# Kernel tuning notes

Hardware: AMD Instinct MI355X
Metric: run time of the kernel (lower is better)

The kernel has to match this reference:

```python
import jax, jax.numpy as jnp
import numpy as np
from jax import lax

NPOINT = 1024
RADIUS = 0.2
NSAMPLE = 32
BN_EPS = 1e-3  # tf_util batch_norm variance_epsilon


def setup_inputs() -> dict:
    key = jax.random.key(0)
    ks = jax.random.split(key, 16)
    B, N, Cp = 8, 4096, 64
    mlp = [64, 64, 128]
    cin = 3 + Cp  # use_xyz=True concatenates local coords
    dk, dout = 128, 128
    inp = {}
    inp["xyz"] = jax.random.uniform(ks[0], (B, N, 3), jnp.float32)
    inp["points"] = jax.random.normal(ks[1], (B, N, Cp), jnp.float32)
    dims = [cin] + mlp
    for i in range(3):
        inp[f"W{i}"] = jax.random.normal(ks[2 + i], (dims[i], dims[i + 1]), jnp.float32) / np.sqrt(dims[i]).astype(np.float32)
        inp[f"b{i}"] = jnp.zeros((dims[i + 1],), jnp.float32)
        inp[f"g{i}"] = jnp.ones((dims[i + 1],), jnp.float32)
        inp[f"be{i}"] = jnp.zeros((dims[i + 1],), jnp.float32)
    inp["Wq"] = jax.random.normal(ks[10], (3, dk), jnp.float32) * 0.1
    inp["Wk"] = jax.random.normal(ks[11], (mlp[-1], dk), jnp.float32) * 0.1
    inp["Wv"] = jax.random.normal(ks[12], (mlp[-1], dout), jnp.float32) * 0.1
    return inp


def farthest_point_sample(xyz, npoint):
    # xyz: [B, N, 3] -> idx [B, npoint] (sequential FPS, seeded at point 0)
    B, N, _ = xyz.shape

    def body(carry, _):
        dist, farthest = carry  # dist [B,N], farthest [B]
        centroid = jnp.take_along_axis(xyz, farthest[:, None, None], axis=1)  # [B,1,3]
        d = jnp.sum((xyz - centroid) ** 2, axis=-1)  # [B,N]
        dist = jnp.minimum(dist, d)
        nxt = jnp.argmax(dist, axis=-1).astype(jnp.int32)
        return (dist, nxt), farthest

    init = (jnp.full((B, N), 1e10, xyz.dtype), jnp.zeros((B,), jnp.int32))
    _, idxs = lax.scan(body, init, None, length=npoint)
    return jnp.transpose(idxs)  # [B, npoint]


def query_ball_point(radius, nsample, xyz, new_xyz):
    # first `nsample` points (in index order) within radius; pad with first hit
    N = xyz.shape[1]
    d2 = jnp.sum((new_xyz[:, :, None, :] - xyz[:, None, :, :]) ** 2, axis=-1)  # [B,S,N]
    inball = d2 < radius * radius
    ar = jnp.arange(N, dtype=jnp.int32)
    order_key = jnp.where(inball, ar, ar + N)
    idx = jnp.argsort(order_key, axis=-1)[..., :nsample].astype(jnp.int32)  # [B,S,nsample]
    valid = jnp.take_along_axis(inball, idx, axis=-1)
    idx = jnp.where(valid, idx, idx[..., :1])
    return idx


def group_point(feat, idx):
    # feat [B,N,C], idx [B,S,K] -> [B,S,K,C]
    return jax.vmap(lambda f, i: f[i])(feat, idx)


def _conv_bn_relu(x, W, b, g, be):
    y = jnp.einsum('bskc,cd->bskd', x, W) + b  # 1x1 conv == pointwise linear
    mean = jnp.mean(y, axis=(0, 1, 2))
    var = jnp.var(y, axis=(0, 1, 2))
    y = (y - mean) * g * lax.rsqrt(var + BN_EPS) + be
    return jax.nn.relu(y)


def _forward(xyz, points, Ws, bs, gs, bes, Wq, Wk, Wv):
    fps_idx = farthest_point_sample(xyz, NPOINT)                 # [B,S]
    new_xyz = jnp.take_along_axis(xyz, fps_idx[..., None], 1)    # [B,S,3]
    idx = query_ball_point(RADIUS, NSAMPLE, xyz, new_xyz)        # [B,S,K]
    grouped_xyz = group_point(xyz, idx) - new_xyz[:, :, None, :]  # local coords
    grouped_pts = group_point(points, idx)
    new_points = jnp.concatenate([grouped_xyz, grouped_pts], axis=-1)  # [B,S,K,3+C]
    for W, b, g, be in zip(Ws, bs, gs, bes):
        new_points = _conv_bn_relu(new_points, W, b, g, be)
    # attention pooling over the K neighbors, query from group center coords
    dk = Wq.shape[1]
    q = new_xyz @ Wq                                         # [B,S,dk]
    k = jnp.einsum('bskc,cd->bskd', new_points, Wk)          # [B,S,K,dk]
    v = jnp.einsum('bskc,co->bsko', new_points, Wv)          # [B,S,K,out]
    scores = jax.nn.softmax(jnp.einsum('bsd,bskd->bsk', q, k) / jnp.sqrt(jnp.float32(dk)), axis=-1)
    pooled = jnp.einsum('bsk,bsko->bso', scores, v)          # [B,S,out]
    return new_xyz, pooled, idx


def reference(xyz, points, W0, b0, g0, be0, W1, b1, g1, be1, W2, b2, g2, be2, Wq, Wk, Wv):
    return _forward(xyz, points, (W0, W1, W2), (b0, b1, b2), (g0, g1, g2), (be0, be1, be2), Wq, Wk, Wv)
```

## Files before the change

kernel.cpp:

```cpp
#include <hip/hip_runtime.h>
#include <hip/hip_bf16.h>

#define DI __device__ __forceinline__

DI float fmulr(float a, float b){ return __fmul_rn(a,b); }
DI float faddr(float a, float b){ return __fadd_rn(a,b); }
DI float fsubr(float a, float b){ return __fsub_rn(a,b); }
DI float dist2e(float x,float y,float z,float cx,float cy,float cz){
  float dx=fsubr(x,cx), dy=fsubr(y,cy), dz=fsubr(z,cz);
  return faddr(faddr(fmulr(dx,dx),fmulr(dy,dy)),fmulr(dz,dz));
}
DI unsigned short f2bf(float f){ __hip_bfloat16 h=__float2bfloat16(f); return *reinterpret_cast<unsigned short*>(&h); }

template<int C> DI float dmax_step(float x){
  int y=__builtin_amdgcn_update_dpp(0, __float_as_int(x), C, 0xF, 0xF, true);
  return fmaxf(x, __int_as_float(y));
}

__global__ __launch_bounds__(256) void fps_kernel(const float* __restrict__ xyz, float* __restrict__ out0){
  __shared__ float4 sp4[4096];
  float* spf=(float*)sp4;
  int* spi=(int*)sp4;
  int b=blockIdx.x, tid=threadIdx.x;
  const float* xb = xyz + (size_t)b*4096*3;
  for(int e=tid;e<12288;e+=256){
    int p=e/3, c=e-3*p;
    spf[4*p+c]=xb[e];
  }
  __syncthreads();
  float px[16],py[16],pz[16],dist[16];
  int p0 = tid*16;
  #pragma unroll
  for(int j=0;j<16;j++){ float4 r=sp4[p0+j]; px[j]=r.x; py[j]=r.y; pz[j]=r.z; dist[j]=1e10f; }
  int cur=0;
  float4 cc0=sp4[0];
  float cx=cc0.x, cy=cc0.y, cz=cc0.z;
  int w=tid>>6, lane=tid&63;
  int c0s=0,c1s=0,c2s=0,c3s=0;
  float* ob = out0 + (size_t)b*1024*3;
  #pragma unroll 1
  for(int t=0;t<1024;t++){
    bool mine = ((t&255)==tid);
    int hi = t>>8;
    c0s = (mine && hi==0) ? cur : c0s;
    c1s = (mine && hi==1) ? cur : c1s;
    c2s = (mine && hi==2) ? cur : c2s;
    c3s = (mine && hi==3) ? cur : c3s;
    float nd[16];
    #pragma unroll
    for(int j=0;j<16;j++){
      float d=dist2e(px[j],py[j],pz[j],cx,cy,cz);
      float m=fminf(dist[j],d); dist[j]=m; nd[j]=m;
    }
    float a0=fmaxf(nd[0],nd[1]), a1=fmaxf(nd[2],nd[3]), a2=fmaxf(nd[4],nd[5]), a3=fmaxf(nd[6],nd[7]);
    float a4=fmaxf(nd[8],nd[9]), a5=fmaxf(nd[10],nd[11]), a6=fmaxf(nd[12],nd[13]), a7=fmaxf(nd[14],nd[15]);
    float b0=fmaxf(a0,a1), b1=fmaxf(a2,a3), b2=fmaxf(a4,a5), b3=fmaxf(a6,a7);
    float bv=fmaxf(fmaxf(b0,b1),fmaxf(b2,b3));
    unsigned msk=0u;
    #pragma unroll
    for(int j=0;j<16;j++) msk |= (nd[j]==bv) ? (1u<<j) : 0u;
    int bj=__ffs(msk)-1;
    int bi=p0+bj;
    float x=bv;
    x=dmax_step<0x111>(x); x=dmax_step<0x112>(x); x=dmax_step<0x114>(x); x=dmax_step<0x118>(x);
    x=dmax_step<0x142>(x); x=dmax_step<0x143>(x);
    float wv=__int_as_float(__builtin_amdgcn_readlane(__float_as_int(x),63));
    unsigned long long em=__ballot(bv==wv);
    int L=(int)(__ffsll(em)-1);
    int wbi=__builtin_amdgcn_readlane(bi,L);
    int par=t&1;
    if(lane==0){
      spf[4*(par*8+w)+3]=wv;
      spi[4*(par*8+4+w)+3]=wbi;
    }
    __syncthreads();
    float w0=spf[4*(par*8+0)+3], w1=spf[4*(par*8+1)+3], w2=spf[4*(par*8+2)+3], w3=spf[4*(par*8+3)+3];
    int   i0=spi[4*(par*8+4)+3], i1=spi[4*(par*8+5)+3], i2=spi[4*(par*8+6)+3], i3=spi[4*(par*8+7)+3];
    float mv=fmaxf(fmaxf(w0,w1),fmaxf(w2,w3));
    int u0=(w0==mv)?i0:0x7fffffff, u1=(w1==mv)?i1:0x7fffffff;
    int u2=(w2==mv)?i2:0x7fffffff, u3=(w3==mv)?i3:0x7fffffff;
    cur=min(min(u0,u1),min(u2,u3));
    float4 cc=sp4[cur]; cx=cc.x; cy=cc.y; cz=cc.z;
  }
  { int t0=tid;     float4 c=sp4[c0s]; ob[t0*3]=c.x; ob[t0*3+1]=c.y; ob[t0*3+2]=c.z; }
  { int t1=tid+256; float4 c=sp4[c1s]; ob[t1*3]=c.x; ob[t1*3+1]=c.y; ob[t1*3+2]=c.z; }
  { int t2=tid+512; float4 c=sp4[c2s]; ob[t2*3]=c.x; ob[t2*3+1]=c.y; ob[t2*3+2]=c.z; }
  { int t3=tid+768; float4 c=sp4[c3s]; ob[t3*3]=c.x; ob[t3*3+1]=c.y; ob[t3*3+2]=c.z; }
}

__global__ __launch_bounds__(256) void ballq_kernel(const float* __restrict__ xyz, const float* __restrict__ out0,
        int* __restrict__ idxw, float* __restrict__ out2){
  __shared__ float sp[12288];
  int tid=threadIdx.x;
  int g = blockIdx.x*4 + (tid>>6);
  int lane = tid&63;
  int b = blockIdx.x>>8;
  const float* xb = xyz + (size_t)b*4096*3;
  const float4* src=(const float4*)xb; float4* dst=(float4*)sp;
  #pragma unroll
  for(int i=0;i<12;i++) dst[i*256+tid]=src[i*256+tid];
  __syncthreads();
  float cx=out0[(size_t)g*3], cy=out0[(size_t)g*3+1], cz=out0[(size_t)g*3+2];
  const float R2 = (float)(0.2*0.2);
  int cnt=0, firstp=0; bool haveFirst=false;
  for(int c=0;c<64;c++){
    int p=c*64+lane;
    float x=sp[3*p], y=sp[3*p+1], z=sp[3*p+2];
    float d2=dist2e(x,y,z,cx,cy,cz);
    bool inb = d2 < R2;
    unsigned long long mask=__ballot(inb);
    if(!haveFirst && mask){ firstp = c*64 + (__ffsll((unsigned long long)mask)-1); haveFirst=true; }
    int pos = cnt + (int)__popcll(mask & ((1ull<<lane)-1ull));
    if(inb && pos<32){ idxw[(size_t)g*32+pos]=p; out2[(size_t)g*32+pos]=(float)p; }
    cnt += (int)__popcll(mask);
    if(cnt>=32) break;
  }
  if(cnt<32){
    for(int j=cnt+lane; j<32; j+=64){ idxw[(size_t)g*32+j]=firstp; out2[(size_t)g*32+j]=(float)firstp; }
  }
}

__global__ void m_kernel(const float* __restrict__ Wq, const float* __restrict__ Wk, float* __restrict__ M){
  int c = threadIdx.x;
  float m0=0.f,m1=0.f,m2=0.f;
  for(int d=0; d<128; d++){
    float wk = Wk[c*128+d];
    m0 += Wq[d]*wk; m1 += Wq[128+d]*wk; m2 += Wq[256+d]*wk;
  }
  M[c]=m0; M[128+c]=m1; M[256+c]=m2;
}

__global__ __launch_bounds__(256) void l0_kernel(const float* __restrict__ xyz, const float* __restrict__ pts,
    const float* __restrict__ out0, const int* __restrict__ idxw,
    const float* __restrict__ W0, const float* __restrict__ b0,
    __hip_bfloat16* __restrict__ y0, float* __restrict__ P){
  __shared__ float xl[64*69];
  int tid=threadIdx.x; int base=blockIdx.x*64;
  int w=tid>>6, lane=tid&63;
  for(int i=0;i<16;i++){
    int r=w*16+i; int R=base+r;
    int g=R>>5; int b=g>>10; int p=idxw[R];
    const float* prow = pts + ((size_t)b*4096 + (size_t)p)*64;
    xl[r*69+3+lane] = prow[lane];
    if(lane<3){
      xl[r*69+lane] = fsubr(xyz[((size_t)b*4096+(size_t)p)*3+lane], out0[(size_t)g*3+lane]);
    }
  }
  __syncthreads();
  int r=tid&63;
  int cgu=__builtin_amdgcn_readfirstlane(tid>>6);
  float acc[16];
  #pragma unroll
  for(int j=0;j<16;j++) acc[j]=b0[cgu*16+j];
  for(int c=0;c<67;c++){
    float xv=xl[r*69+c];
    #pragma unroll
    for(int j=0;j<16;j++) acc[j] += xv*W0[c*64+cgu*16+j];
  }
  size_t R=(size_t)base+r;
  unsigned short tb[16];
  #pragma unroll
  for(int j=0;j<16;j++) tb[j]=f2bf(acc[j]);
  uint4* ov=(uint4*)(y0 + R*64 + cgu*16);
  ov[0]=make_uint4(tb[0]|(tb[1]<<16), tb[2]|(tb[3]<<16), tb[4]|(tb[5]<<16), tb[6]|(tb[7]<<16));
  ov[1]=make_uint4(tb[8]|(tb[9]<<16), tb[10]|(tb[11]<<16), tb[12]|(tb[13]<<16), tb[14]|(tb[15]<<16));
  #pragma unroll
  for(int j=0;j<16;j++){
    float s=acc[j], q=acc[j]*acc[j];
    #pragma unroll
    for(int m=32;m>=1;m>>=1){ s+=__shfl_xor(s,m); q+=__shfl_xor(q,m); }
    if(r==0){ P[(size_t)(cgu*16+j)*4096 + blockIdx.x]=s; P[(size_t)(128+cgu*16+j)*4096 + blockIdx.x]=q; }
  }
}

template<int CIN,int COUT>
__global__ __launch_bounds__(256) void lmid_kernel(const __hip_bfloat16* __restrict__ xin,
    const float* __restrict__ ssIn, const float* __restrict__ W, const float* __restrict__ bias,
    __hip_bfloat16* __restrict__ yout, float* __restrict__ P){
  constexpr int STR=CIN+1;
  constexpr int PER=COUT/4;
  __shared__ float xl[64*STR];
  int tid=threadIdx.x; size_t base=(size_t)blockIdx.x*64;
  constexpr int CHUNKS = 64*CIN/8;
  #pragma unroll
  for(int i=0;i<CHUNKS/256;i++){
    int e=i*256+tid;
    int r=e/(CIN/8), c0=(e%(CIN/8))*8;
    uint4 raw = *reinterpret_cast<const uint4*>(xin + (base+(size_t)r)*CIN + c0);
    unsigned u[4]={raw.x,raw.y,raw.z,raw.w};
    #pragma unroll
    for(int k=0;k<4;k++){
      int c=c0+2*k;
      float lo=__uint_as_float(u[k]<<16);
      float hi=__uint_as_float(u[k]&0xFFFF0000u);
      float a=lo*ssIn[c]+ssIn[128+c];
      float bq=hi*ssIn[c+1]+ssIn[128+c+1];
      xl[r*STR+c]  = a>0.f?a:0.f;
      xl[r*STR+c+1]= bq>0.f?bq:0.f;
    }
  }
  __syncthreads();
  int r=tid&63;
  int cgu=__builtin_amdgcn_readfirstlane(tid>>6);
  float acc[PER];
  #pragma unroll
  for(int j=0;j<PER;j++) acc[j]=bias[cgu*PER+j];
  for(int c=0;c<CIN;c++){
    float xv=xl[r*STR+c];
    #pragma unroll
    for(int j=0;j<PER;j++) acc[j] += xv*W[c*COUT+cgu*PER+j];
  }
  size_t R=base+r;
  unsigned short tb[PER];
  #pragma unroll
  for(int j=0;j<PER;j++) tb[j]=f2bf(acc[j]);
  uint4* ov=(uint4*)(yout + R*COUT + cgu*PER);
  #pragma unroll
  for(int v=0;v<PER/8;v++)
    ov[v]=make_uint4(tb[v*8]|(tb[v*8+1]<<16), tb[v*8+2]|(tb[v*8+3]<<16), tb[v*8+4]|(tb[v*8+5]<<16), tb[v*8+6]|(tb[v*8+7]<<16));
  #pragma unroll
  for(int j=0;j<PER;j++){
    float s=acc[j],q=acc[j]*acc[j];
    #pragma unroll
    for(int m=32;m>=1;m>>=1){s+=__shfl_xor(s,m);q+=__shfl_xor(q,m);}
    if(r==0){ P[(size_t)(cgu*PER+j)*4096 + blockIdx.x]=s; P[(size_t)(128+cgu*PER+j)*4096 + blockIdx.x]=q; }
  }
}

__global__ void fin_kernel(const float* __restrict__ P, const float* __restrict__ gg, const float* __restrict__ be,
                           float* __restrict__ ss){
  int ch=blockIdx.x; int lane=threadIdx.x;
  float s=0.f,q=0.f;
  for(int blk=lane; blk<4096; blk+=64){ s+=P[(size_t)ch*4096+blk]; q+=P[(size_t)(128+ch)*4096+blk]; }
  #pragma unroll
  for(int m=32;m>=1;m>>=1){ s+=__shfl_xor(s,m); q+=__shfl_xor(q,m); }
  if(lane==0){
    const float invNT = 1.0f/262144.0f;
    float mean=s*invNT; float var=q*invNT - mean*mean;
    float scale=gg[ch]/sqrtf(var+1e-3f);
    ss[ch]=scale; ss[128+ch]=be[ch]-mean*scale;
  }
}

__global__ __launch_bounds__(256) void sh_kernel(const __hip_bfloat16* __restrict__ y2,
    const float* __restrict__ ss2, const float* __restrict__ M, const float* __restrict__ out0,
    float* __restrict__ hbar){
  __shared__ float h[2][32*130];
  __shared__ float uLds[2][128];
  __shared__ float sLds[2][32];
  int tid=threadIdx.x; int grp=tid>>7, t=tid&127;
  size_t g=(size_t)blockIdx.x*2+grp;
  #pragma unroll
  for(int i=0;i<4;i++){
    int e=i*128+t;
    int row=e>>4, c0=(e&15)*8;
    uint4 raw=*reinterpret_cast<const uint4*>(y2+(g*32+(size_t)row)*128+c0);
    unsigned u[4]={raw.x,raw.y,raw.z,raw.w};
    #pragma unroll
    for(int k=0;k<4;k++){
      int c=c0+2*k;
      float lo=__uint_as_float(u[k]<<16), hi=__uint_as_float(u[k]&0xFFFF0000u);
      float a=lo*ss2[c]+ss2[128+c]; float bq=hi*ss2[c+1]+ss2[128+c+1];
      h[grp][row*130+c]  = a>0.f?a:0.f;
      h[grp][row*130+c+1]= bq>0.f?bq:0.f;
    }
  }
  float cx=out0[g*3], cy=out0[g*3+1], cz=out0[g*3+2];
  uLds[grp][t]=cx*M[t]+cy*M[128+t]+cz*M[256+t];
  __syncthreads();
  if(t<32){
    float sc=0.f;
    for(int c=0;c<128;c++) sc+=h[grp][t*130+c]*uLds[grp][c];
    sc*=0.08838834764831845f;
    float mx=sc;
    #pragma unroll
    for(int m=16;m>=1;m>>=1) mx=fmaxf(mx,__shfl_xor(mx,m));
    float p=expf(sc-mx);
    float sum=p;
    #pragma unroll
    for(int m=16;m>=1;m>>=1) sum+=__shfl_xor(sum,m);
    sLds[grp][t]=p/sum;
  }
  __syncthreads();
  float hb=0.f;
  for(int k=0;k<32;k++) hb+=sLds[grp][k]*h[grp][k*130+t];
  hbar[g*128+t]=hb;
}

__global__ __launch_bounds__(256) void pool_kernel(const float* __restrict__ hbar, const float* __restrict__ Wv,
    float* __restrict__ out1){
  __shared__ float xl[32*129];
  int tid=threadIdx.x; size_t g0=(size_t)blockIdx.x*32;
  for(int e=tid;e<32*128;e+=256){ int r=e>>7,ch=e&127; xl[r*129+ch]=hbar[(g0+(size_t)r)*128+ch]; }
  __syncthreads();
  int r=tid&31;
  int cgu=__builtin_amdgcn_readfirstlane(tid>>5);
  float acc[16];
  #pragma unroll
  for(int j=0;j<16;j++) acc[j]=0.f;
  for(int c=0;c<128;c++){
    float xv=xl[r*129+c];
    #pragma unroll
    for(int j=0;j<16;j++) acc[j]+=xv*Wv[c*128+cgu*16+j];
  }
  #pragma unroll
  for(int j=0;j<16;j++) out1[(g0+(size_t)r)*128+cgu*16+j]=acc[j];
}

extern "C" void kernel_launch(void* const* d_in, const int* in_sizes, int n_in,
                              void* d_out, int out_size, void* d_ws, size_t ws_size,
                              hipStream_t stream){
  (void)in_sizes; (void)n_in; (void)out_size; (void)ws_size;
  const float* xyz=(const float*)d_in[0];
  const float* pts=(const float*)d_in[1];
  const float* W0=(const float*)d_in[2];  const float* b0=(const float*)d_in[3];
  const float* g0=(const float*)d_in[4];  const float* be0=(const float*)d_in[5];
  const float* W1=(const float*)d_in[6];  const float* b1=(const float*)d_in[7];
  const float* g1=(const float*)d_in[8];  const float* be1=(const float*)d_in[9];
  const float* W2=(const float*)d_in[10]; const float* b2=(const float*)d_in[11];
  const float* g2=(const float*)d_in[12]; const float* be2=(const float*)d_in[13];
  const float* Wq=(const float*)d_in[14]; const float* Wk=(const float*)d_in[15];
  const float* Wv=(const float*)d_in[16];
  float* out0=(float*)d_out;
  float* out1=out0 + (size_t)8*1024*3;
  float* out2=out1 + (size_t)8192*128;

  char* ws=(char*)d_ws; size_t off=0;
  int* idxw=(int*)(ws+off);                    off += (size_t)8192*32*4;
  __hip_bfloat16* fa=(__hip_bfloat16*)(ws+off); off += (size_t)262144*64*2;
  __hip_bfloat16* fb=(__hip_bfloat16*)(ws+off); off += (size_t)262144*64*2;
  __hip_bfloat16* fc=(__hip_bfloat16*)(ws+off); off += (size_t)262144*128*2;
  float* P =(float*)(ws+off);                  off += (size_t)256*4096*4;
  float* ss0=(float*)(ws+off);                 off += 256*4;
  float* ss1=(float*)(ws+off);                 off += 256*4;
  float* ss2=(float*)(ws+off);                 off += 256*4;
  float* M =(float*)(ws+off);                  off += 3*128*4 + 128;
  float* hb=(float*)(ws+off);                  off += (size_t)8192*128*4;

  hipLaunchKernelGGL(fps_kernel,   dim3(8),    dim3(256),  0, stream, xyz, out0);
  hipLaunchKernelGGL(ballq_kernel, dim3(2048), dim3(256),  0, stream, xyz, out0, idxw, out2);
  hipLaunchKernelGGL(m_kernel,     dim3(1),    dim3(128),  0, stream, Wq, Wk, M);
  hipLaunchKernelGGL(l0_kernel,    dim3(4096), dim3(256),  0, stream, xyz, pts, out0, idxw, W0, b0, fa, P);
  hipLaunchKernelGGL(fin_kernel,   dim3(64),   dim3(64),   0, stream, P, g0, be0, ss0);
  hipLaunchKernelGGL((lmid_kernel<64,64>),  dim3(4096), dim3(256), 0, stream, fa, ss0, W1, b1, fb, P);
  hipLaunchKernelGGL(fin_kernel,   dim3(64),   dim3(64),   0, stream, P, g1, be1, ss1);
  hipLaunchKernelGGL((lmid_kernel<64,128>), dim3(4096), dim3(256), 0, stream, fb, ss1, W2, b2, fc, P);
  hipLaunchKernelGGL(fin_kernel,   dim3(128),  dim3(64),   0, stream, P, g2, be2, ss2);
  hipLaunchKernelGGL(sh_kernel,    dim3(4096), dim3(256),  0, stream, fc, ss2, M, out0, hb);
  hipLaunchKernelGGL(pool_kernel,  dim3(256),  dim3(256),  0, stream, hb, Wv, out1);
}
```

Before: 970.7 us.

## Vectorize FPS distance update with packed float2 and pack argmax keys

The FPS inner loop now holds point coordinates in two-wide float vectors, so distance and min/max updates can map to packed FP32 instructions. FP contraction is turned off to keep results bitwise identical to the reference. The cross-wave argmax reduction packs value and inverted index into one 64-bit key in dedicated shared slots, replacing separate value and index reads and the tie-break logic with a plain integer max. Separately, the sh_kernel score dot product is split across four thread groups with partial sums in shared memory instead of 32 threads each looping over 128 channels, at the cost of an extra barrier.

```diff
diff --git a/kernel.cpp b/kernel.cpp
--- a/kernel.cpp
+++ b/kernel.cpp
@@ -2,6 +2,8 @@
 #include <hip/hip_bf16.h>
 
 #define DI __device__ __forceinline__
+
+typedef float v2f __attribute__((ext_vector_type(2)));
 
 DI float fmulr(float a, float b){ return __fmul_rn(a,b); }
 DI float faddr(float a, float b){ return __fadd_rn(a,b); }
@@ -18,9 +20,10 @@
 }
 
 __global__ __launch_bounds__(256) void fps_kernel(const float* __restrict__ xyz, float* __restrict__ out0){
-  __shared__ float4 sp4[4096];
-  float* spf=(float*)sp4;
-  int* spi=(int*)sp4;
+  extern __shared__ char smem[];
+  float4* sp4=(float4*)smem;
+  float* spf=(float*)smem;
+  unsigned long long* slots=(unsigned long long*)(smem+65536);
   int b=blockIdx.x, tid=threadIdx.x;
   const float* xb = xyz + (size_t)b*4096*3;
   for(int e=tid;e<12288;e+=256){
@@ -28,10 +31,14 @@
     spf[4*p+c]=xb[e];
   }
   __syncthreads();
-  float px[16],py[16],pz[16],dist[16];
-  int p0 = tid*16;
-  #pragma unroll
-  for(int j=0;j<16;j++){ float4 r=sp4[p0+j]; px[j]=r.x; py[j]=r.y; pz[j]=r.z; dist[j]=1e10f; }
+  v2f px[8],py[8],pz[8],dist[8];
+  int p0=tid*16;
+  #pragma unroll
+  for(int j=0;j<8;j++){
+    float4 r0=sp4[p0+2*j], r1=sp4[p0+2*j+1];
+    px[j]=(v2f){r0.x,r1.x}; py[j]=(v2f){r0.y,r1.y}; pz[j]=(v2f){r0.z,r1.z};
+    dist[j]=(v2f){1e10f,1e10f};
+  }
   int cur=0;
   float4 cc0=sp4[0];
   float cx=cc0.x, cy=cc0.y, cz=cc0.z;
@@ -40,25 +47,38 @@
   float* ob = out0 + (size_t)b*1024*3;
   #pragma unroll 1
   for(int t=0;t<1024;t++){
-    bool mine = ((t&255)==tid);
-    int hi = t>>8;
-    c0s = (mine && hi==0) ? cur : c0s;
-    c1s = (mine && hi==1) ? cur : c1s;
-    c2s = (mine && hi==2) ? cur : c2s;
-    c3s = (mine && hi==3) ? cur : c3s;
-    float nd[16];
-    #pragma unroll
-    for(int j=0;j<16;j++){
-      float d=dist2e(px[j],py[j],pz[j],cx,cy,cz);
-      float m=fminf(dist[j],d); dist[j]=m; nd[j]=m;
-    }
-    float a0=fmaxf(nd[0],nd[1]), a1=fmaxf(nd[2],nd[3]), a2=fmaxf(nd[4],nd[5]), a3=fmaxf(nd[6],nd[7]);
-    float a4=fmaxf(nd[8],nd[9]), a5=fmaxf(nd[10],nd[11]), a6=fmaxf(nd[12],nd[13]), a7=fmaxf(nd[14],nd[15]);
-    float b0=fmaxf(a0,a1), b1=fmaxf(a2,a3), b2=fmaxf(a4,a5), b3=fmaxf(a6,a7);
-    float bv=fmaxf(fmaxf(b0,b1),fmaxf(b2,b3));
+    bool mine=((t&255)==tid);
+    int hi=t>>8;
+    c0s=(mine&&hi==0)?cur:c0s;
+    c1s=(mine&&hi==1)?cur:c1s;
+    c2s=(mine&&hi==2)?cur:c2s;
+    c3s=(mine&&hi==3)?cur:c3s;
+    v2f nd[8];
+    {
+      #pragma clang fp contract(off)
+      v2f c2x={cx,cx}, c2y={cy,cy}, c2z={cz,cz};
+      #pragma unroll
+      for(int j=0;j<8;j++){
+        v2f dx=px[j]-c2x, dy=py[j]-c2y, dz=pz[j]-c2z;
+        v2f dd=(dx*dx+dy*dy)+dz*dz;
+        v2f nm=__builtin_elementwise_min(dist[j],dd);
+        dist[j]=nm; nd[j]=nm;
+      }
+    }
+    v2f e0=__builtin_elementwise_max(nd[0],nd[1]);
+    v2f e1=__builtin_elementwise_max(nd[2],nd[3]);
+    v2f e2=__builtin_elementwise_max(nd[4],nd[5]);
+    v2f e3=__builtin_elementwise_max(nd[6],nd[7]);
+    v2f f0=__builtin_elementwise_max(e0,e1);
+    v2f f1=__builtin_elementwise_max(e2,e3);
+    v2f g =__builtin_elementwise_max(f0,f1);
+    float bv=fmaxf(g.x,g.y);
     unsigned msk=0u;
     #pragma unroll
-    for(int j=0;j<16;j++) msk |= (nd[j]==bv) ? (1u<<j) : 0u;
+    for(int j=0;j<8;j++){
+      msk |= (nd[j].x==bv)?(1u<<(2*j)):0u;
+      msk |= (nd[j].y==bv)?(1u<<(2*j+1)):0u;
+    }
     int bj=__ffs(msk)-1;
     int bi=p0+bj;
     float x=bv;
@@ -70,16 +90,16 @@
     int wbi=__builtin_amdgcn_readlane(bi,L);
     int par=t&1;
     if(lane==0){
-      spf[4*(par*8+w)+3]=wv;
-      spi[4*(par*8+4+w)+3]=wbi;
+      slots[par*4+w] = ((unsigned long long)__float_as_uint(wv)<<32)
+                     | (unsigned long long)(0xFFFFFFFFu-(unsigned)wbi);
     }
     __syncthreads();
-    float w0=spf[4*(par*8+0)+3], w1=spf[4*(par*8+1)+3], w2=spf[4*(par*8+2)+3], w3=spf[4*(par*8+3)+3];
-    int   i0=spi[4*(par*8+4)+3], i1=spi[4*(par*8+5)+3], i2=spi[4*(par*8+6)+3], i3=spi[4*(par*8+7)+3];
-    float mv=fmaxf(fmaxf(w0,w1),fmaxf(w2,w3));
-    int u0=(w0==mv)?i0:0x7fffffff, u1=(w1==mv)?i1:0x7fffffff;
-    int u2=(w2==mv)?i2:0x7fffffff, u3=(w3==mv)?i3:0x7fffffff;
-    cur=min(min(u0,u1),min(u2,u3));
+    const ulonglong2* sl2=(const ulonglong2*)(slots+par*4);
+    ulonglong2 ka=sl2[0], kb=sl2[1];
+    unsigned long long m0 = ka.x>ka.y?ka.x:ka.y;
+    unsigned long long m1 = kb.x>kb.y?kb.x:kb.y;
+    unsigned long long k  = m0>m1?m0:m1;
+    cur=(int)(0xFFFFFFFFu-(unsigned)(k&0xFFFFFFFFull));
     float4 cc=sp4[cur]; cx=cc.x; cy=cc.y; cz=cc.z;
   }
   { int t0=tid;     float4 c=sp4[c0s]; ob[t0*3]=c.x; ob[t0*3+1]=c.y; ob[t0*3+2]=c.z; }
@@ -248,6 +268,7 @@
   __shared__ float h[2][32*130];
   __shared__ float uLds[2][128];
   __shared__ float sLds[2][32];
+  __shared__ float partLds[2][4][32];
   int tid=threadIdx.x; int grp=tid>>7, t=tid&127;
   size_t g=(size_t)blockIdx.x*2+grp;
   #pragma unroll
@@ -268,14 +289,23 @@
   float cx=out0[g*3], cy=out0[g*3+1], cz=out0[g*3+2];
   uLds[grp][t]=cx*M[t]+cy*M[128+t]+cz*M[256+t];
   __syncthreads();
+  {
+    int row=t&31, q=t>>5;
+    float sc=0.f;
+    const float* hr=&h[grp][row*130];
+    const float* ur=&uLds[grp][0];
+    #pragma unroll
+    for(int c=0;c<32;c++) sc += hr[q*32+c]*ur[q*32+c];
+    partLds[grp][q][row]=sc;
+  }
+  __syncthreads();
   if(t<32){
-    float sc=0.f;
-    for(int c=0;c<128;c++) sc+=h[grp][t*130+c]*uLds[grp][c];
-    sc*=0.08838834764831845f;
-    float mx=sc;
+    float s=(partLds[grp][0][t]+partLds[grp][1][t])+(partLds[grp][2][t]+partLds[grp][3][t]);
+    s*=0.08838834764831845f;
+    float mx=s;
     #pragma unroll
     for(int m=16;m>=1;m>>=1) mx=fmaxf(mx,__shfl_xor(mx,m));
-    float p=expf(sc-mx);
+    float p=expf(s-mx);
     float sum=p;
     #pragma unroll
     for(int m=16;m>=1;m>>=1) sum+=__shfl_xor(sum,m);
@@ -337,7 +367,7 @@
   float* M =(float*)(ws+off);                  off += 3*128*4 + 128;
   float* hb=(float*)(ws+off);                  off += (size_t)8192*128*4;
 
-  hipLaunchKernelGGL(fps_kernel,   dim3(8),    dim3(256),  0, stream, xyz, out0);
+  hipLaunchKernelGGL(fps_kernel,   dim3(8),    dim3(256), 65536+64, stream, xyz, out0);
   hipLaunchKernelGGL(ballq_kernel, dim3(2048), dim3(256),  0, stream, xyz, out0, idxw, out2);
   hipLaunchKernelGGL(m_kernel,     dim3(1),    dim3(128),  0, stream, Wq, Wk, M);
   hipLaunchKernelGGL(l0_kernel,    dim3(4096), dim3(256),  0, stream, xyz, pts, out0, idxw, W0, b0, fa, P);
```

New measurement: 984.2 us. No clear change (+1.4%).

## Use bf16 MFMA for middle MLP layers and split score dot product

Applied to the files above, without the earlier changes.

Replaces the scalar FP32 per-thread matmul in the middle conv layers with bf16 MFMA 16x16x32 instructions. Activations are normalised, passed through ReLU and rounded to bf16 in LDS, and the weights are transposed into LDS as bf16. Outputs are staged in LDS so global stores are coalesced, and the batch-norm partial sums are reduced through LDS. The attention score dot product in sh_kernel is also split across all 128 threads instead of 32, using a partial-sum buffer. Rounding inputs and weights to bf16 adds precision loss, and every block pays a per-block weight transpose into LDS.

```diff
diff --git a/kernel.cpp b/kernel.cpp
--- a/kernel.cpp
+++ b/kernel.cpp
@@ -2,6 +2,10 @@
 #include <hip/hip_bf16.h>
 
 #define DI __device__ __forceinline__
+
+typedef float v2f __attribute__((ext_vector_type(2)));
+typedef __attribute__((ext_vector_type(8))) short bf16x8;
+typedef __attribute__((ext_vector_type(4))) float f32x4;
 
 DI float fmulr(float a, float b){ return __fmul_rn(a,b); }
 DI float faddr(float a, float b){ return __fadd_rn(a,b); }
@@ -174,56 +178,77 @@
 }
 
 template<int CIN,int COUT>
-__global__ __launch_bounds__(256) void lmid_kernel(const __hip_bfloat16* __restrict__ xin,
+__global__ __launch_bounds__(256) void lmid_mfma(const __hip_bfloat16* __restrict__ xin,
     const float* __restrict__ ssIn, const float* __restrict__ W, const float* __restrict__ bias,
     __hip_bfloat16* __restrict__ yout, float* __restrict__ P){
-  constexpr int STR=CIN+1;
-  constexpr int PER=COUT/4;
-  __shared__ float xl[64*STR];
+  constexpr int XS = CIN+8;
+  constexpr int YS = COUT+8;
+  constexpr int NT = COUT/16;
+  __shared__ unsigned short xt[64*XS];
+  __shared__ unsigned short wt[COUT*XS];
+  __shared__ unsigned short yt[64*YS];
+  __shared__ float ps[4][COUT];
+  __shared__ float qs[4][COUT];
   int tid=threadIdx.x; size_t base=(size_t)blockIdx.x*64;
-  constexpr int CHUNKS = 64*CIN/8;
-  #pragma unroll
-  for(int i=0;i<CHUNKS/256;i++){
-    int e=i*256+tid;
+  int w=tid>>6, lane=tid&63;
+  for(int e=tid; e<64*CIN/8; e+=256){
     int r=e/(CIN/8), c0=(e%(CIN/8))*8;
     uint4 raw = *reinterpret_cast<const uint4*>(xin + (base+(size_t)r)*CIN + c0);
     unsigned u[4]={raw.x,raw.y,raw.z,raw.w};
-    #pragma unroll
-    for(int k=0;k<4;k++){
-      int c=c0+2*k;
-      float lo=__uint_as_float(u[k]<<16);
-      float hi=__uint_as_float(u[k]&0xFFFF0000u);
-      float a=lo*ssIn[c]+ssIn[128+c];
-      float bq=hi*ssIn[c+1]+ssIn[128+c+1];
-      xl[r*STR+c]  = a>0.f?a:0.f;
-      xl[r*STR+c+1]= bq>0.f?bq:0.f;
-    }
-  }
-  __syncthreads();
-  int r=tid&63;
-  int cgu=__builtin_amdgcn_readfirstlane(tid>>6);
-  float acc[PER];
-  #pragma unroll
-  for(int j=0;j<PER;j++) acc[j]=bias[cgu*PER+j];
-  for(int c=0;c<CIN;c++){
-    float xv=xl[r*STR+c];
-    #pragma unroll
-    for(int j=0;j<PER;j++) acc[j] += xv*W[c*COUT+cgu*PER+j];
-  }
-  size_t R=base+r;
-  unsigned short tb[PER];
-  #pragma unroll
-  for(int j=0;j<PER;j++) tb[j]=f2bf(acc[j]);
-  uint4* ov=(uint4*)(yout + R*COUT + cgu*PER);
-  #pragma unroll
-  for(int v=0;v<PER/8;v++)
-    ov[v]=make_uint4(tb[v*8]|(tb[v*8+1]<<16), tb[v*8+2]|(tb[v*8+3]<<16), tb[v*8+4]|(tb[v*8+5]<<16), tb[v*8+6]|(tb[v*8+7]<<16));
-  #pragma unroll
-  for(int j=0;j<PER;j++){
-    float s=acc[j],q=acc[j]*acc[j];
-    #pragma unroll
-    for(int m=32;m>=1;m>>=1){s+=__shfl_xor(s,m);q+=__shfl_xor(q,m);}
-    if(r==0){ P[(size_t)(cgu*PER+j)*4096 + blockIdx.x]=s; P[(size_t)(128+cgu*PER+j)*4096 + blockIdx.x]=q; }
+    unsigned short* dst=&xt[r*XS+c0];
+    #pragma unroll
+    for(int k2=0;k2<4;k2++){
+      int c=c0+2*k2;
+      float lo=__uint_as_float(u[k2]<<16);
+      float hi=__uint_as_float(u[k2]&0xFFFF0000u);
+      float a=lo*ssIn[c]+ssIn[128+c]; a=a>0.f?a:0.f;
+      float bq=hi*ssIn[c+1]+ssIn[128+c+1]; bq=bq>0.f?bq:0.f;
+      dst[2*k2]=f2bf(a); dst[2*k2+1]=f2bf(bq);
+    }
+  }
+  for(int e=tid; e<CIN*COUT; e+=256){
+    int k=e/COUT, n=e-k*COUT;
+    wt[n*XS+k]=f2bf(W[e]);
+  }
+  __syncthreads();
+  f32x4 acc[NT];
+  #pragma unroll
+  for(int t=0;t<NT;t++) acc[t]=(f32x4){0.f,0.f,0.f,0.f};
+  int m=lane&15, kg=lane>>4;
+  #pragma unroll
+  for(int ks=0; ks<CIN/32; ks++){
+    int k0=ks*32+kg*8;
+    bf16x8 af = *(bf16x8*)&xt[(w*16+m)*XS + k0];
+    #pragma unroll
+    for(int t=0;t<NT;t++){
+      bf16x8 bfr = *(bf16x8*)&wt[(t*16+m)*XS + k0];
+      acc[t]=__builtin_amdgcn_mfma_f32_16x16x32_bf16(af,bfr,acc[t],0,0,0);
+    }
+  }
+  #pragma unroll
+  for(int t=0;t<NT;t++){
+    float bv=bias[t*16+m];
+    float s=0.f,q=0.f;
+    #pragma unroll
+    for(int rg=0;rg<4;rg++){
+      float v=acc[t][rg]+bv;
+      s+=v; q+=v*v;
+      yt[(w*16+kg*4+rg)*YS + t*16+m]=f2bf(v);
+    }
+    s+=__shfl_xor(s,16); q+=__shfl_xor(q,16);
+    s+=__shfl_xor(s,32); q+=__shfl_xor(q,32);
+    if(kg==0){ ps[w][t*16+m]=s; qs[w][t*16+m]=q; }
+  }
+  __syncthreads();
+  if(tid<COUT){
+    float s=ps[0][tid]+ps[1][tid]+ps[2][tid]+ps[3][tid];
+    float q=qs[0][tid]+qs[1][tid]+qs[2][tid]+qs[3][tid];
+    P[(size_t)tid*4096+blockIdx.x]=s;
+    P[(size_t)(128+tid)*4096+blockIdx.x]=q;
+  }
+  for(int e=tid; e<64*COUT/8; e+=256){
+    int r=e/(COUT/8), c0=(e%(COUT/8))*8;
+    *reinterpret_cast<uint4*>(yout + (base+(size_t)r)*COUT + c0) = *reinterpret_cast<uint4*>(&yt[r*YS+c0]);
   }
 }
 
@@ -248,6 +273,7 @@
   __shared__ float h[2][32*130];
   __shared__ float uLds[2][128];
   __shared__ float sLds[2][32];
+  __shared__ float partLds[2][4][32];
   int tid=threadIdx.x; int grp=tid>>7, t=tid&127;
   size_t g=(size_t)blockIdx.x*2+grp;
   #pragma unroll
@@ -268,14 +294,23 @@
   float cx=out0[g*3], cy=out0[g*3+1], cz=out0[g*3+2];
   uLds[grp][t]=cx*M[t]+cy*M[128+t]+cz*M[256+t];
   __syncthreads();
+  {
+    int row=t&31, q=t>>5;
+    float sc=0.f;
+    const float* hr=&h[grp][row*130];
+    const float* ur=&uLds[grp][0];
+    #pragma unroll
+    for(int c=0;c<32;c++) sc += hr[q*32+c]*ur[q*32+c];
+    partLds[grp][q][row]=sc;
+  }
+  __syncthreads();
   if(t<32){
-    float sc=0.f;
-    for(int c=0;c<128;c++) sc+=h[grp][t*130+c]*uLds[grp][c];
-    sc*=0.08838834764831845f;
-    float mx=sc;
+    float s=(partLds[grp][0][t]+partLds[grp][1][t])+(partLds[grp][2][t]+partLds[grp][3][t]);
+    s*=0.08838834764831845f;
+    float mx=s;
     #pragma unroll
     for(int m=16;m>=1;m>>=1) mx=fmaxf(mx,__shfl_xor(mx,m));
-    float p=expf(sc-mx);
+    float p=expf(s-mx);
     float sum=p;
     #pragma unroll
     for(int m=16;m>=1;m>>=1) sum+=__shfl_xor(sum,m);
@@ -342,9 +377,9 @@
   hipLaunchKernelGGL(m_kernel,     dim3(1),    dim3(128),  0, stream, Wq, Wk, M);
   hipLaunchKernelGGL(l0_kernel,    dim3(4096), dim3(256),  0, stream, xyz, pts, out0, idxw, W0, b0, fa, P);
   hipLaunchKernelGGL(fin_kernel,   dim3(64),   dim3(64),   0, stream, P, g0, be0, ss0);
-  hipLaunchKernelGGL((lmid_kernel<64,64>),  dim3(4096), dim3(256), 0, stream, fa, ss0, W1, b1, fb, P);
+  hipLaunchKernelGGL((lmid_mfma<64,64>),  dim3(4096), dim3(256), 0, stream, fa, ss0, W1, b1, fb, P);
   hipLaunchKernelGGL(fin_kernel,   dim3(64),   dim3(64),   0, stream, P, g1, be1, ss1);
-  hipLaunchKernelGGL((lmid_kernel<64,128>), dim3(4096), dim3(256), 0, stream, fb, ss1, W2, b2, fc, P);
+  hipLaunchKernelGGL((lmid_mfma<64,128>), dim3(4096), dim3(256), 0, stream, fb, ss1, W2, b2, fc, P);
   hipLaunchKernelGGL(fin_kernel,   dim3(128),  dim3(64),   0, stream, P, g2, be2, ss2);
   hipLaunchKernelGGL(sh_kernel,    dim3(4096), dim3(256),  0, stream, fc, ss2, M, out0, hb);
   hipLaunchKernelGGL(pool_kernel,  dim3(256),  dim3(256),  0, stream, hb, Wv, out1);
```

New measurement: 888.0 us. 1.09x faster.
